# Optimization experiments

Measured on AMD Instinct MI355X. Metric: run time of the kernel, lower is better.

The kernel has to match this reference:

```python
import jax, jax.numpy as jnp
import numpy as np

D_MODEL = 1024
N_HEADS = 16
D_K = 64

def setup_inputs() -> dict:
    key = jax.random.key(0)
    k0, k1, k2, k3, k4 = jax.random.split(key, 5)
    B, S = 4, 4096
    std = 0.02
    x = jax.random.normal(k0, (B, S, D_MODEL), dtype=jnp.float32)
    # nn.Linear weights are [out, in]; init normal(0, 0.02) as in _init_weights
    W_q = std * jax.random.normal(k1, (N_HEADS * D_K, D_MODEL), dtype=jnp.float32)
    W_k = std * jax.random.normal(k2, (N_HEADS * D_K, D_MODEL), dtype=jnp.float32)
    W_v = std * jax.random.normal(k3, (N_HEADS * D_K, D_MODEL), dtype=jnp.float32)
    W_o = std * jax.random.normal(k4, (D_MODEL, N_HEADS * D_K), dtype=jnp.float32)
    return {"x": x, "W_q": W_q, "W_k": W_k, "W_v": W_v, "W_o": W_o}

def reference(x, W_q, W_k, W_v, W_o):
    B, S, _ = x.shape
    H, Dk = N_HEADS, D_K
    # projections (nn.Linear: x @ W.T), reshape to [B, S, H, Dk]
    q = (x @ W_q.T).reshape(B, S, H, Dk)
    k = (x @ W_k.T).reshape(B, S, H, Dk)
    v = (x @ W_v.T).reshape(B, S, H, Dk)
    scale = 1.0 / jnp.sqrt(jnp.float32(Dk))
    # No softmax between the two matmuls -> reassociate (QK^T)V = Q(K^TV),
    # identical math, O(S*d^2) instead of O(S^2*d).
    kv = jnp.einsum('bshd,bshe->bhde', k, v)          # [B, H, Dk, Dk]
    attn = jnp.einsum('bshd,bhde->bshe', q, kv) * scale  # [B, S, H, Dk]
    out = attn.reshape(B, S, H * Dk) @ W_o.T
    return out
```

## Files before the change

### kernel.cpp

```cpp
#include <hip/hip_runtime.h>
#include <hip/hip_bf16.h>
#include <cstdint>


typedef __bf16 bf16x8 __attribute__((ext_vector_type(8)));
typedef float f32x4 __attribute__((ext_vector_type(4)));
typedef unsigned short ushort_t;

__device__ inline void gld_lds16(const void* g, void* l) {
    __builtin_amdgcn_global_load_lds(
        (const __attribute__((address_space(1))) unsigned int*)g,
        (__attribute__((address_space(3))) unsigned int*)l,
        16, 0, 0);
}

__device__ inline ushort_t f2bf(float f) {
    uint32_t u = __float_as_uint(f);
    uint32_t r = (u + 0x7fffu + ((u >> 16) & 1u)) >> 16;
    return (ushort_t)r;
}

template <typename OutT>
__global__ __launch_bounds__(256, 2)
void gemm_bt(const ushort_t* __restrict__ A, int lda, long strideA,
             const ushort_t* __restrict__ B, int ldb, long strideB,
             OutT* __restrict__ C0, int ldc0, long strideC0,
             OutT* __restrict__ C1, int ldc1, long strideC1, int nsplit,
             int K)
{
    __shared__ ushort_t lA[128 * 32];
    __shared__ ushort_t lB[128 * 32];

    const int t    = threadIdx.x;
    const int lane = t & 63;
    const int wid  = t >> 6;

    A += (size_t)blockIdx.z * strideA;
    B += (size_t)blockIdx.z * strideB;

    const int m0 = blockIdx.x * 128;
    const int n0 = blockIdx.y * 128;

    const int wm = (wid >> 1) * 64;
    const int wn = (wid & 1) * 64;
    const int mr = lane & 15;
    const int q4 = lane >> 4;

    const int row_a = t >> 2;
    const int seg   = ((t & 3) ^ ((t >> 3) & 3)) * 8;

    const int csw = (q4 ^ ((mr >> 1) & 3)) * 16;

    f32x4 acc[4][4] = {};

    for (int k0 = 0; k0 < K; k0 += 32) {
        __syncthreads();
        gld_lds16(A + (size_t)(m0 + row_a) * lda + k0 + seg,      (char*)lA + wid * 1024);
        gld_lds16(A + (size_t)(m0 + 64 + row_a) * lda + k0 + seg, (char*)lA + 4096 + wid * 1024);
        gld_lds16(B + (size_t)(n0 + row_a) * ldb + k0 + seg,      (char*)lB + wid * 1024);
        gld_lds16(B + (size_t)(n0 + 64 + row_a) * ldb + k0 + seg, (char*)lB + 4096 + wid * 1024);
        __syncthreads();

        bf16x8 af[4], bf[4];
#pragma unroll
        for (int i = 0; i < 4; ++i)
            af[i] = *(const bf16x8*)((const char*)lA + (wm + i * 16 + mr) * 64 + csw);
#pragma unroll
        for (int j = 0; j < 4; ++j)
            bf[j] = *(const bf16x8*)((const char*)lB + (wn + j * 16 + mr) * 64 + csw);
#pragma unroll
        for (int i = 0; i < 4; ++i)
#pragma unroll
            for (int j = 0; j < 4; ++j)
                acc[i][j] = __builtin_amdgcn_mfma_f32_16x16x32_bf16(af[i], bf[j], acc[i][j], 0, 0, 0);
    }

    OutT* Cw; int ldcw, nc0;
    if (n0 < nsplit) { Cw = C0 + (size_t)blockIdx.z * strideC0; ldcw = ldc0; nc0 = n0; }
    else             { Cw = C1 + (size_t)blockIdx.z * strideC1; ldcw = ldc1; nc0 = n0 - nsplit; }

#pragma unroll
    for (int i = 0; i < 4; ++i) {
        const int rbase = m0 + wm + i * 16 + q4 * 4;
#pragma unroll
        for (int j = 0; j < 4; ++j) {
            const int col = nc0 + wn + j * 16 + mr;
#pragma unroll
            for (int r = 0; r < 4; ++r) {
                const float v = acc[i][j][r];
                const size_t off = (size_t)(rbase + r) * ldcw + col;
                if constexpr (sizeof(OutT) == 2) Cw[off] = f2bf(v);
                else                             Cw[off] = v;
            }
        }
    }
}

__global__ __launch_bounds__(256)
void kv_kernel(const ushort_t* __restrict__ KVslab, int ld,
               float* __restrict__ KVp)
{
    __shared__ ushort_t sK[32 * 64];
    __shared__ ushort_t sV[32 * 64];

    const int t  = threadIdx.x;
    const int bh = blockIdx.y;
    const int b  = bh >> 4, h = bh & 15;
    const int s_base = blockIdx.x * 256;

    const ushort_t* Kp = KVslab + (size_t)(b * 4096) * ld + h * 64;
    const ushort_t* Vp = Kp + 1024;

    const int d0 = (t >> 4) * 4;
    const int e0 = (t & 15) * 4;
    float acc[4][4] = {};

    const int lrow = t >> 3;
    const int lcol = (t & 7) * 8;

    for (int c = 0; c < 8; ++c) {
        const int s0 = s_base + c * 32;
        __syncthreads();
        *(uint4*)&sK[lrow * 64 + lcol] = *(const uint4*)&Kp[(size_t)(s0 + lrow) * ld + lcol];
        *(uint4*)&sV[lrow * 64 + lcol] = *(const uint4*)&Vp[(size_t)(s0 + lrow) * ld + lcol];
        __syncthreads();
#pragma unroll 8
        for (int s = 0; s < 32; ++s) {
            const uint2 kk = *(const uint2*)&sK[s * 64 + d0];
            const uint2 vv = *(const uint2*)&sV[s * 64 + e0];
            float kd[4], ve[4];
            kd[0] = __uint_as_float(kk.x << 16);
            kd[1] = __uint_as_float(kk.x & 0xffff0000u);
            kd[2] = __uint_as_float(kk.y << 16);
            kd[3] = __uint_as_float(kk.y & 0xffff0000u);
            ve[0] = __uint_as_float(vv.x << 16);
            ve[1] = __uint_as_float(vv.x & 0xffff0000u);
            ve[2] = __uint_as_float(vv.y << 16);
            ve[3] = __uint_as_float(vv.y & 0xffff0000u);
#pragma unroll
            for (int i = 0; i < 4; ++i)
#pragma unroll
                for (int j = 0; j < 4; ++j)
                    acc[i][j] += kd[i] * ve[j];
        }
    }

    float* outp = KVp + ((size_t)(blockIdx.x * 64 + bh)) * 4096;
#pragma unroll
    for (int i = 0; i < 4; ++i) {
        float4 o; o.x = acc[i][0]; o.y = acc[i][1]; o.z = acc[i][2]; o.w = acc[i][3];
        *(float4*)&outp[(d0 + i) * 64 + e0] = o;
    }
}

__global__ __launch_bounds__(256)
void reduce_kv(const float4* __restrict__ in, float4* __restrict__ out)
{
    const int i = blockIdx.x * 256 + threadIdx.x;
    float4 a = in[i];
#pragma unroll
    for (int s = 1; s < 16; ++s) {
        const float4 b = in[s * 65536 + i];
        a.x += b.x; a.y += b.y; a.z += b.z; a.w += b.w;
    }
    out[i] = a;
}

__global__ __launch_bounds__(256)
void make_E(const float* __restrict__ KV, const float* __restrict__ Wo,
            ushort_t* __restrict__ Et)
{
    __shared__ float skv[64 * 65];
    __shared__ float swo[64 * 65];

    const int t  = threadIdx.x;
    const int bh = blockIdx.y;
    const int b  = bh >> 4, h = bh & 15;
    const int j0 = blockIdx.x * 64;

    const float* kvp = KV + (size_t)bh * 4096;
#pragma unroll
    for (int i = 0; i < 4; ++i) {
        const int idx = t + i * 256;
        const int r = idx >> 4, c = (idx & 15) * 4;
        const float4 f = *(const float4*)&kvp[r * 64 + c];
        skv[r * 65 + c + 0] = f.x;
        skv[r * 65 + c + 1] = f.y;
        skv[r * 65 + c + 2] = f.z;
        skv[r * 65 + c + 3] = f.w;
        const float4 g = *(const float4*)&Wo[(size_t)(j0 + r) * 1024 + h * 64 + c];
        swo[r * 65 + c + 0] = g.x;
        swo[r * 65 + c + 1] = g.y;
        swo[r * 65 + c + 2] = g.z;
        swo[r * 65 + c + 3] = g.w;
    }
    __syncthreads();

    const int d0 = (t & 15) * 4;
#pragma unroll
    for (int pass = 0; pass < 4; ++pass) {
        const int jloc = (t >> 4) + pass * 16;
        float s0 = 0.f, s1 = 0.f, s2 = 0.f, s3 = 0.f;
        const float* wrow = &swo[jloc * 65];
#pragma unroll 8
        for (int e = 0; e < 64; ++e) {
            const float w = wrow[e];
            s0 += skv[(d0 + 0) * 65 + e] * w;
            s1 += skv[(d0 + 1) * 65 + e] * w;
            s2 += skv[(d0 + 2) * 65 + e] * w;
            s3 += skv[(d0 + 3) * 65 + e] * w;
        }
        ushort4 o;
        o.x = f2bf(s0 * 0.125f);
        o.y = f2bf(s1 * 0.125f);
        o.z = f2bf(s2 * 0.125f);
        o.w = f2bf(s3 * 0.125f);
        *(ushort4*)&Et[((size_t)b * 1024 + j0 + jloc) * 1024 + h * 64 + d0] = o;
    }
}

__global__ __launch_bounds__(256)
void cast_bf16(const float* __restrict__ in, ushort_t* __restrict__ out, int n)
{
    const int i = (blockIdx.x * 256 + threadIdx.x) * 4;
    if (i >= n) return;
    const float4 f = *(const float4*)&in[i];
    ushort4 o;
    o.x = f2bf(f.x); o.y = f2bf(f.y); o.z = f2bf(f.z); o.w = f2bf(f.w);
    *(ushort4*)&out[i] = o;
}

__global__ __launch_bounds__(256)
void cast_w3(const float* __restrict__ a, const float* __restrict__ b,
             const float* __restrict__ c, ushort_t* __restrict__ out)
{
    const float* src = (blockIdx.y == 0) ? a : (blockIdx.y == 1) ? b : c;
    const int i = (blockIdx.x * 256 + threadIdx.x) * 4;
    const float4 f = *(const float4*)&src[i];
    ushort4 o;
    o.x = f2bf(f.x); o.y = f2bf(f.y); o.z = f2bf(f.z); o.w = f2bf(f.w);
    *(ushort4*)&out[(size_t)blockIdx.y * 1048576 + i] = o;
}


extern "C" void kernel_launch(void* const* d_in, const int* in_sizes, int n_in,
                              void* d_out, int out_size, void* d_ws, size_t ws_size,
                              hipStream_t stream)
{
    const float* x  = (const float*)d_in[0];
    const float* Wq = (const float*)d_in[1];
    const float* Wk = (const float*)d_in[2];
    const float* Wv = (const float*)d_in[3];
    const float* Wo = (const float*)d_in[4];
    float* out = (float*)d_out;

    const int B = 4, S = 4096, D = 1024;
    const int M  = B * S;
    const int N3 = 3 * D;

    char* ws = (char*)d_ws;
    size_t off = 0;
    auto alloc = [&](size_t bytes) -> void* {
        void* p = ws + off;
        off += (bytes + 255) & ~(size_t)255;
        return p;
    };
    ushort_t* xb     = (ushort_t*)alloc((size_t)M * D * 2);
    ushort_t* qb     = (ushort_t*)alloc((size_t)M * D * 2);
    ushort_t* kvslab = (ushort_t*)alloc((size_t)M * 2 * D * 2);
    ushort_t* wqkv   = (ushort_t*)alloc((size_t)N3 * D * 2);
    float*    kvr    = (float*)alloc((size_t)64 * 4096 * 4);
    float*    kvp = (float*)xb;
    ushort_t* Et  = xb;

    cast_bf16<<<dim3((M * D) / 4 / 256), dim3(256), 0, stream>>>(x, xb, M * D);
    cast_w3<<<dim3((D * D) / 4 / 256, 3), dim3(256), 0, stream>>>(Wq, Wk, Wv, wqkv);

    gemm_bt<ushort_t><<<dim3(M / 128, N3 / 128, 1), dim3(256), 0, stream>>>(
        xb, D, 0, wqkv, D, 0,
        qb, D, 0, kvslab, 2 * D, 0, D, D);

    kv_kernel<<<dim3(16, 64), dim3(256), 0, stream>>>(kvslab, 2 * D, kvp);
    reduce_kv<<<dim3(256), dim3(256), 0, stream>>>((const float4*)kvp, (float4*)kvr);

    make_E<<<dim3(16, 64), dim3(256), 0, stream>>>(kvr, Wo, Et);

    gemm_bt<float><<<dim3(S / 128, D / 128, B), dim3(256), 0, stream>>>(
        qb, D, (long)S * D, Et, D, (long)D * D,
        out, D, (long)S * D, (float*)nullptr, 0, 0, 1 << 30, D);
}
```

Measured before the change: 368.9 us.

## Reassociate projections via per-batch Gram matrix X^T X to cut GEMM work

Instead of projecting Q, K and V over all tokens, computes the Gram matrix X^T X per batch (split-K, then reduced), derives K^T V through Wk·G·Wv^T, and folds Wq into the output weight so the final step is a single GEMM on x. This removes the large QKV projection GEMM and the K/V intermediate traffic. The cost is a transposed copy of x, bf16 partial Gram buffers with extra reduction kernels, and more rounding steps.

```diff
diff --git a/kernel.cpp b/kernel.cpp
--- a/kernel.cpp
+++ b/kernel.cpp
@@ -18,6 +18,9 @@
     uint32_t u = __float_as_uint(f);
     uint32_t r = (u + 0x7fffu + ((u >> 16) & 1u)) >> 16;
     return (ushort_t)r;
+}
+__device__ inline float bf2f(ushort_t u) {
+    return __uint_as_float((uint32_t)u << 16);
 }
 
 template <typename OutT>
@@ -26,7 +29,7 @@
              const ushort_t* __restrict__ B, int ldb, long strideB,
              OutT* __restrict__ C0, int ldc0, long strideC0,
              OutT* __restrict__ C1, int ldc1, long strideC1, int nsplit,
-             int K)
+             int K, int kslices)
 {
     __shared__ ushort_t lA[128 * 32];
     __shared__ ushort_t lB[128 * 32];
@@ -35,8 +38,13 @@
     const int lane = t & 63;
     const int wid  = t >> 6;
 
-    A += (size_t)blockIdx.z * strideA;
-    B += (size_t)blockIdx.z * strideB;
+    const int z = blockIdx.z;
+    int bb, ks;
+    if (kslices == 4) { bb = z >> 2; ks = z & 3; }
+    else              { bb = z;      ks = 0;     }
+
+    A += (size_t)bb * strideA + (size_t)ks * K;
+    B += (size_t)bb * strideB + (size_t)ks * K;
 
     const int m0 = blockIdx.x * 128;
     const int n0 = blockIdx.y * 128;
@@ -48,8 +56,7 @@
 
     const int row_a = t >> 2;
     const int seg   = ((t & 3) ^ ((t >> 3) & 3)) * 8;
-
-    const int csw = (q4 ^ ((mr >> 1) & 3)) * 16;
+    const int csw   = (q4 ^ ((mr >> 1) & 3)) * 16;
 
     f32x4 acc[4][4] = {};
 
@@ -76,8 +83,8 @@
     }
 
     OutT* Cw; int ldcw, nc0;
-    if (n0 < nsplit) { Cw = C0 + (size_t)blockIdx.z * strideC0; ldcw = ldc0; nc0 = n0; }
-    else             { Cw = C1 + (size_t)blockIdx.z * strideC1; ldcw = ldc1; nc0 = n0 - nsplit; }
+    if (n0 < nsplit) { Cw = C0 + (size_t)z * strideC0; ldcw = ldc0; nc0 = n0; }
+    else             { Cw = C1 + (size_t)z * strideC1; ldcw = ldc1; nc0 = n0 - nsplit; }
 
 #pragma unroll
     for (int i = 0; i < 4; ++i) {
@@ -97,55 +104,157 @@
 }
 
 __global__ __launch_bounds__(256)
-void kv_kernel(const ushort_t* __restrict__ KVslab, int ld,
-               float* __restrict__ KVp)
-{
-    __shared__ ushort_t sK[32 * 64];
-    __shared__ ushort_t sV[32 * 64];
-
+void cast_x_t(const float* __restrict__ x, ushort_t* __restrict__ xb,
+              ushort_t* __restrict__ xbT)
+{
+    __shared__ ushort_t lt[64 * 66];
     const int t  = threadIdx.x;
+    const int s0 = blockIdx.x * 64;
+    const int i0 = blockIdx.y * 64;
+
+#pragma unroll
+    for (int c = 0; c < 4; ++c) {
+        const int idx = c * 256 + t;
+        const int r = idx >> 4, c4 = (idx & 15) * 4;
+        const float4 f = *(const float4*)&x[(size_t)(s0 + r) * 1024 + i0 + c4];
+        ushort4 o;
+        o.x = f2bf(f.x); o.y = f2bf(f.y); o.z = f2bf(f.z); o.w = f2bf(f.w);
+        *(ushort4*)&xb[(size_t)(s0 + r) * 1024 + i0 + c4] = o;
+        *(uint32_t*)&lt[r * 66 + c4]     = (uint32_t)o.x | ((uint32_t)o.y << 16);
+        *(uint32_t*)&lt[r * 66 + c4 + 2] = (uint32_t)o.z | ((uint32_t)o.w << 16);
+    }
+    __syncthreads();
+#pragma unroll
+    for (int c = 0; c < 4; ++c) {
+        const int idx = c * 256 + t;
+        const int ri = idx >> 4, s4 = (idx & 15) * 4;
+        ushort4 o;
+        o.x = lt[(s4 + 0) * 66 + ri];
+        o.y = lt[(s4 + 1) * 66 + ri];
+        o.z = lt[(s4 + 2) * 66 + ri];
+        o.w = lt[(s4 + 3) * 66 + ri];
+        *(ushort4*)&xbT[(size_t)(i0 + ri) * 16384 + s0 + s4] = o;
+    }
+}
+
+__global__ __launch_bounds__(256)
+void cast_wt(const float* __restrict__ W, ushort_t* __restrict__ WT)
+{
+    __shared__ ushort_t lt[64 * 66];
+    const int t  = threadIdx.x;
+    const int r0 = blockIdx.x * 64;
+    const int c0 = blockIdx.y * 64;
+
+#pragma unroll
+    for (int c = 0; c < 4; ++c) {
+        const int idx = c * 256 + t;
+        const int r = idx >> 4, c4 = (idx & 15) * 4;
+        const float4 f = *(const float4*)&W[(size_t)(r0 + r) * 1024 + c0 + c4];
+        ushort4 o;
+        o.x = f2bf(f.x); o.y = f2bf(f.y); o.z = f2bf(f.z); o.w = f2bf(f.w);
+        *(uint32_t*)&lt[r * 66 + c4]     = (uint32_t)o.x | ((uint32_t)o.y << 16);
+        *(uint32_t*)&lt[r * 66 + c4 + 2] = (uint32_t)o.z | ((uint32_t)o.w << 16);
+    }
+    __syncthreads();
+#pragma unroll
+    for (int c = 0; c < 4; ++c) {
+        const int idx = c * 256 + t;
+        const int ri = idx >> 4, s4 = (idx & 15) * 4;
+        ushort4 o;
+        o.x = lt[(s4 + 0) * 66 + ri];
+        o.y = lt[(s4 + 1) * 66 + ri];
+        o.z = lt[(s4 + 2) * 66 + ri];
+        o.w = lt[(s4 + 3) * 66 + ri];
+        *(ushort4*)&WT[(size_t)(c0 + ri) * 1024 + r0 + s4] = o;
+    }
+}
+
+__global__ __launch_bounds__(256)
+void cast_w2(const float* __restrict__ a, const float* __restrict__ b,
+             ushort_t* __restrict__ out)
+{
+    const float* src = (blockIdx.y == 0) ? a : b;
+    const int i = (blockIdx.x * 256 + threadIdx.x) * 4;
+    const float4 f = *(const float4*)&src[i];
+    ushort4 o;
+    o.x = f2bf(f.x); o.y = f2bf(f.y); o.z = f2bf(f.z); o.w = f2bf(f.w);
+    *(ushort4*)&out[(size_t)blockIdx.y * 1048576 + i] = o;
+}
+
+__global__ __launch_bounds__(256)
+void reduce_g(const ushort4* __restrict__ Gp, ushort4* __restrict__ G)
+{
+    const int gid = blockIdx.x * 256 + threadIdx.x;
+    const int b = gid >> 18, r = gid & 262143;
+    float s0 = 0.f, s1 = 0.f, s2 = 0.f, s3 = 0.f;
+#pragma unroll
+    for (int ks = 0; ks < 4; ++ks) {
+        const ushort4 u = Gp[(size_t)(b * 4 + ks) * 262144 + r];
+        s0 += bf2f(u.x); s1 += bf2f(u.y); s2 += bf2f(u.z); s3 += bf2f(u.w);
+    }
+    ushort4 o;
+    o.x = f2bf(s0); o.y = f2bf(s1); o.z = f2bf(s2); o.w = f2bf(s3);
+    G[gid] = o;
+}
+
+__global__ __launch_bounds__(256)
+void kvblk(const ushort_t* __restrict__ H, const ushort_t* __restrict__ Wv,
+           float* __restrict__ KVp)
+{
+    __shared__ ushort_t sH[64 * 132];
+    __shared__ ushort_t sV[64 * 132];
+
+    const int t  = threadIdx.x;
+    const int is = blockIdx.x;
     const int bh = blockIdx.y;
     const int b  = bh >> 4, h = bh & 15;
-    const int s_base = blockIdx.x * 256;
-
-    const ushort_t* Kp = KVslab + (size_t)(b * 4096) * ld + h * 64;
-    const ushort_t* Vp = Kp + 1024;
+
+    const ushort_t* Hp = H + ((size_t)b << 20) + (size_t)(h * 64) * 1024 + is * 128;
+    const ushort_t* Vp = Wv + (size_t)(h * 64) * 1024 + is * 128;
+
+#pragma unroll
+    for (int i2 = 0; i2 < 8; ++i2) {
+        const int ci = i2 * 256 + t;
+        const int r = ci >> 5, c = (ci & 31) * 4;
+        *(uint2*)&sH[r * 132 + c] = *(const uint2*)&Hp[(size_t)r * 1024 + c];
+        *(uint2*)&sV[r * 132 + c] = *(const uint2*)&Vp[(size_t)r * 1024 + c];
+    }
+    __syncthreads();
 
     const int d0 = (t >> 4) * 4;
     const int e0 = (t & 15) * 4;
     float acc[4][4] = {};
 
-    const int lrow = t >> 3;
-    const int lcol = (t & 7) * 8;
-
-    for (int c = 0; c < 8; ++c) {
-        const int s0 = s_base + c * 32;
-        __syncthreads();
-        *(uint4*)&sK[lrow * 64 + lcol] = *(const uint4*)&Kp[(size_t)(s0 + lrow) * ld + lcol];
-        *(uint4*)&sV[lrow * 64 + lcol] = *(const uint4*)&Vp[(size_t)(s0 + lrow) * ld + lcol];
-        __syncthreads();
-#pragma unroll 8
-        for (int s = 0; s < 32; ++s) {
-            const uint2 kk = *(const uint2*)&sK[s * 64 + d0];
-            const uint2 vv = *(const uint2*)&sV[s * 64 + e0];
-            float kd[4], ve[4];
-            kd[0] = __uint_as_float(kk.x << 16);
-            kd[1] = __uint_as_float(kk.x & 0xffff0000u);
-            kd[2] = __uint_as_float(kk.y << 16);
-            kd[3] = __uint_as_float(kk.y & 0xffff0000u);
-            ve[0] = __uint_as_float(vv.x << 16);
-            ve[1] = __uint_as_float(vv.x & 0xffff0000u);
-            ve[2] = __uint_as_float(vv.y << 16);
-            ve[3] = __uint_as_float(vv.y & 0xffff0000u);
-#pragma unroll
-            for (int i = 0; i < 4; ++i)
-#pragma unroll
-                for (int j = 0; j < 4; ++j)
-                    acc[i][j] += kd[i] * ve[j];
+#pragma unroll 2
+    for (int i4 = 0; i4 < 128; i4 += 4) {
+        uint2 hu[4], vu[4];
+#pragma unroll
+        for (int j = 0; j < 4; ++j) {
+            hu[j] = *(const uint2*)&sH[(d0 + j) * 132 + i4];
+            vu[j] = *(const uint2*)&sV[(e0 + j) * 132 + i4];
         }
-    }
-
-    float* outp = KVp + ((size_t)(blockIdx.x * 64 + bh)) * 4096;
+        float hf[4][4], vf[4][4];
+#pragma unroll
+        for (int j = 0; j < 4; ++j) {
+            hf[j][0] = __uint_as_float(hu[j].x << 16);
+            hf[j][1] = __uint_as_float(hu[j].x & 0xffff0000u);
+            hf[j][2] = __uint_as_float(hu[j].y << 16);
+            hf[j][3] = __uint_as_float(hu[j].y & 0xffff0000u);
+            vf[j][0] = __uint_as_float(vu[j].x << 16);
+            vf[j][1] = __uint_as_float(vu[j].x & 0xffff0000u);
+            vf[j][2] = __uint_as_float(vu[j].y << 16);
+            vf[j][3] = __uint_as_float(vu[j].y & 0xffff0000u);
+        }
+#pragma unroll
+        for (int ii = 0; ii < 4; ++ii)
+#pragma unroll
+            for (int di = 0; di < 4; ++di)
+#pragma unroll
+                for (int ej = 0; ej < 4; ++ej)
+                    acc[di][ej] += hf[di][ii] * vf[ej][ii];
+    }
+
+    float* outp = KVp + ((size_t)(is * 64 + bh)) * 4096;
 #pragma unroll
     for (int i = 0; i < 4; ++i) {
         float4 o; o.x = acc[i][0]; o.y = acc[i][1]; o.z = acc[i][2]; o.w = acc[i][3];
@@ -154,12 +263,12 @@
 }
 
 __global__ __launch_bounds__(256)
-void reduce_kv(const float4* __restrict__ in, float4* __restrict__ out)
+void reduce_kv8(const float4* __restrict__ in, float4* __restrict__ out)
 {
     const int i = blockIdx.x * 256 + threadIdx.x;
     float4 a = in[i];
 #pragma unroll
-    for (int s = 1; s < 16; ++s) {
+    for (int s = 1; s < 8; ++s) {
         const float4 b = in[s * 65536 + i];
         a.x += b.x; a.y += b.y; a.z += b.z; a.w += b.w;
     }
@@ -219,29 +328,6 @@
     }
 }
 
-__global__ __launch_bounds__(256)
-void cast_bf16(const float* __restrict__ in, ushort_t* __restrict__ out, int n)
-{
-    const int i = (blockIdx.x * 256 + threadIdx.x) * 4;
-    if (i >= n) return;
-    const float4 f = *(const float4*)&in[i];
-    ushort4 o;
-    o.x = f2bf(f.x); o.y = f2bf(f.y); o.z = f2bf(f.z); o.w = f2bf(f.w);
-    *(ushort4*)&out[i] = o;
-}
-
-__global__ __launch_bounds__(256)
-void cast_w3(const float* __restrict__ a, const float* __restrict__ b,
-             const float* __restrict__ c, ushort_t* __restrict__ out)
-{
-    const float* src = (blockIdx.y == 0) ? a : (blockIdx.y == 1) ? b : c;
-    const int i = (blockIdx.x * 256 + threadIdx.x) * 4;
-    const float4 f = *(const float4*)&src[i];
-    ushort4 o;
-    o.x = f2bf(f.x); o.y = f2bf(f.y); o.z = f2bf(f.z); o.w = f2bf(f.w);
-    *(ushort4*)&out[(size_t)blockIdx.y * 1048576 + i] = o;
-}
-
 
 extern "C" void kernel_launch(void* const* d_in, const int* in_sizes, int n_in,
                               void* d_out, int out_size, void* d_ws, size_t ws_size,
@@ -255,8 +341,7 @@
     float* out = (float*)d_out;
 
     const int B = 4, S = 4096, D = 1024;
-    const int M  = B * S;
-    const int N3 = 3 * D;
+    const long MB1 = 1048576;
 
     char* ws = (char*)d_ws;
     size_t off = 0;
@@ -265,27 +350,44 @@
         off += (bytes + 255) & ~(size_t)255;
         return p;
     };
-    ushort_t* xb     = (ushort_t*)alloc((size_t)M * D * 2);
-    ushort_t* qb     = (ushort_t*)alloc((size_t)M * D * 2);
-    ushort_t* kvslab = (ushort_t*)alloc((size_t)M * 2 * D * 2);
-    ushort_t* wqkv   = (ushort_t*)alloc((size_t)N3 * D * 2);
-    float*    kvr    = (float*)alloc((size_t)64 * 4096 * 4);
-    float*    kvp = (float*)xb;
-    ushort_t* Et  = xb;
-
-    cast_bf16<<<dim3((M * D) / 4 / 256), dim3(256), 0, stream>>>(x, xb, M * D);
-    cast_w3<<<dim3((D * D) / 4 / 256, 3), dim3(256), 0, stream>>>(Wq, Wk, Wv, wqkv);
-
-    gemm_bt<ushort_t><<<dim3(M / 128, N3 / 128, 1), dim3(256), 0, stream>>>(
-        xb, D, 0, wqkv, D, 0,
-        qb, D, 0, kvslab, 2 * D, 0, D, D);
-
-    kv_kernel<<<dim3(16, 64), dim3(256), 0, stream>>>(kvslab, 2 * D, kvp);
-    reduce_kv<<<dim3(256), dim3(256), 0, stream>>>((const float4*)kvp, (float4*)kvr);
+    ushort_t* xb   = (ushort_t*)alloc((size_t)B * S * D * 2);
+    ushort_t* xbT  = (ushort_t*)alloc((size_t)D * B * S * 2);
+    ushort_t* wkv  = (ushort_t*)alloc((size_t)2 * D * D * 2);
+    ushort_t* wqT  = (ushort_t*)alloc((size_t)D * D * 2);
+    ushort_t* Gb   = (ushort_t*)alloc((size_t)B * D * D * 2);
+    float*    kvp  = (float*)alloc((size_t)8 * 64 * 4096 * 4);
+    float*    kvr  = (float*)alloc((size_t)64 * 4096 * 4);
+    char*     R1   = (char*)alloc((size_t)16 * MB1 * 2);
+    ushort_t* Gp = (ushort_t*)R1;
+    ushort_t* Hb = (ushort_t*)R1;
+    ushort_t* Et = (ushort_t*)(R1 + 8 * MB1 * 2);
+    ushort_t* Fb = (ushort_t*)(R1 + 16 * MB1 * 2 - 8 * MB1 * 2);
+    ushort_t* wkb = wkv;
+    ushort_t* wvb = wkv + MB1;
+
+    cast_x_t<<<dim3(256, 16), dim3(256), 0, stream>>>(x, xb, xbT);
+    cast_w2<<<dim3(1024, 2), dim3(256), 0, stream>>>(Wk, Wv, wkv);
+    cast_wt<<<dim3(16, 16), dim3(256), 0, stream>>>(Wq, wqT);
+
+    gemm_bt<ushort_t><<<dim3(8, 8, 16), dim3(256), 0, stream>>>(
+        xbT, 16384, 4096, xbT, 16384, 4096,
+        Gp, D, MB1, (ushort_t*)nullptr, 0, 0, 1 << 30, D, 4);
+    reduce_g<<<dim3(4096), dim3(256), 0, stream>>>((const ushort4*)Gp, (ushort4*)Gb);
+
+    gemm_bt<ushort_t><<<dim3(8, 8, 4), dim3(256), 0, stream>>>(
+        wkb, D, 0, Gb, D, MB1,
+        Hb, D, MB1, (ushort_t*)nullptr, 0, 0, 1 << 30, D, 1);
+
+    kvblk<<<dim3(8, 64), dim3(256), 0, stream>>>(Hb, wvb, kvp);
+    reduce_kv8<<<dim3(256), dim3(256), 0, stream>>>((const float4*)kvp, (float4*)kvr);
 
     make_E<<<dim3(16, 64), dim3(256), 0, stream>>>(kvr, Wo, Et);
 
-    gemm_bt<float><<<dim3(S / 128, D / 128, B), dim3(256), 0, stream>>>(
-        qb, D, (long)S * D, Et, D, (long)D * D,
-        out, D, (long)S * D, (float*)nullptr, 0, 0, 1 << 30, D);
-}
+    gemm_bt<ushort_t><<<dim3(8, 8, 4), dim3(256), 0, stream>>>(
+        Et, D, MB1, wqT, D, 0,
+        Fb, D, MB1, (ushort_t*)nullptr, 0, 0, 1 << 30, D, 1);
+
+    gemm_bt<float><<<dim3(32, 8, 4), dim3(256), 0, stream>>>(
+        xb, D, (long)S * D, Fb, D, MB1,
+        out, D, (long)S * D, (float*)nullptr, 0, 0, 1 << 30, D, 1);
+}
```

Measured after the change: 339.5 us. -8.0%, faster.
